# Kernel optimization log

Measured on AMD Instinct MI355X. Metric: run time of the kernel, lower is better.

## Reference

```python
import jax, jax.numpy as jnp
import numpy as np

N = 8192
E = 262144
DIN = 512
DOUT = 256


def setup_inputs() -> dict:
    key = jax.random.key(0)
    k1, k2, k3, k4 = jax.random.split(key, 4)
    x = jax.random.normal(k1, (N, DIN), dtype=jnp.float32)
    edge_index = jax.random.randint(k2, (2, E), 0, N, dtype=jnp.int64)
    edge_weight = jax.random.uniform(k3, (E,), dtype=jnp.float32)
    W = jax.random.normal(k4, (DOUT, DIN), dtype=jnp.float32) * (1.0 / np.sqrt(DIN))
    return {"x": x, "edge_index": edge_index, "edge_weight": edge_weight, "W": W}


def reference(x, edge_index, edge_weight, W):
    n = x.shape[0]
    # Linear(dim_in, dim_out, bias=False): h = x @ W.T  -> [N, DOUT]
    h = x @ W.T
    # Dense adjacency: A[src, dst] += w (to_dense_adj sums duplicate edges)
    src, dst = edge_index[0], edge_index[1]
    A = jnp.zeros((n, n), dtype=x.dtype).at[src, dst].add(edge_weight)
    # degree from A BEFORE self-loops, then +1 from the added eye on degree_matrix
    deg = jnp.sum(A, axis=1) + 1.0
    # sqrt(inverse(diag(deg))) == diag(1/sqrt(deg)); apply as row scaling
    dinv_sqrt = 1.0 / jnp.sqrt(deg)  # [N]
    A = A + jnp.eye(n, dtype=x.dtype)  # self-loops on adjacency
    # x = D^{-1/2} @ (A.T @ (D^{-1/2} @ h))
    h = dinv_sqrt[:, None] * h
    h = A.T @ h
    h = dinv_sqrt[:, None] * h
    return h
```

## Files before the change

kernel.cpp:

```cpp
#include <hip/hip_runtime.h>

static constexpr int DIN = 512;
static constexpr int DOUT = 256;
static constexpr int CAP = 128;

typedef __attribute__((ext_vector_type(8))) short short8;
typedef __attribute__((ext_vector_type(4))) float f32x4;

__device__ inline unsigned short f2bf(float f) {
  unsigned int b = __float_as_uint(f);
  unsigned int r = (b + 0x7fffu + ((b >> 16) & 1u)) >> 16;
  return (unsigned short)r;
}
__device__ inline float bf_lo(unsigned int packed) { return __uint_as_float(packed << 16); }
__device__ inline float bf_hi(unsigned int packed) { return __uint_as_float(packed & 0xffff0000u); }

__device__ inline short8 cvt8(const float4 a, const float4 b) {
  short8 o;
  o[0] = (short)f2bf(a.x); o[1] = (short)f2bf(a.y);
  o[2] = (short)f2bf(a.z); o[3] = (short)f2bf(a.w);
  o[4] = (short)f2bf(b.x); o[5] = (short)f2bf(b.y);
  o[6] = (short)f2bf(b.z); o[7] = (short)f2bf(b.w);
  return o;
}

__global__ __launch_bounds__(256) void k_setup(
    const float* __restrict__ x, const float* __restrict__ W,
    unsigned short* __restrict__ xb, unsigned short* __restrict__ wbb,
    float* __restrict__ deg, int* __restrict__ cursor, int n, long XT, long WT) {
  long gid = (long)blockIdx.x * 256 + threadIdx.x;
  if (gid < XT) {
    const float4* src = (const float4*)(x + gid * 8);
    float4 a = src[0], b = src[1];
    *(short8*)(xb + gid * 8) = cvt8(a, b);
  } else if (gid < XT + WT) {
    long i = gid - XT;
    const float4* src = (const float4*)(W + i * 8);
    float4 a = src[0], b = src[1];
    *(short8*)(wbb + i * 8) = cvt8(a, b);
  } else {
    long i = gid - XT - WT;
    if (i < n) { deg[i] = 1.0f; cursor[i] = 0; }
  }
}

__global__ __launch_bounds__(256) void k_edges(
    const int* __restrict__ ei, const float* __restrict__ ew,
    float* __restrict__ deg, int* __restrict__ cursor,
    uint2* __restrict__ bucket, int E) {
  int e = blockIdx.x * blockDim.x + threadIdx.x;
  if (e < E) {
    int srcv = ei[e];
    int dstv = ei[E + e];
    float w = ew[e];
    atomicAdd(&deg[srcv], w);
    int pos = atomicAdd(&cursor[dstv], 1);
    if (pos < CAP) {
      uint2 v;
      v.x = (unsigned)srcv;
      v.y = __float_as_uint(w);
      bucket[(size_t)dstv * CAP + pos] = v;
    }
  }
}

__global__ __launch_bounds__(256) void k_gemm_mfma(
    const unsigned short* __restrict__ xb, const unsigned short* __restrict__ wbb,
    const float* __restrict__ deg, unsigned short* __restrict__ h1b) {
  const int lane = threadIdx.x & 63;
  const int wv = threadIdx.x >> 6;
  const int bm = blockIdx.x * 16;
  const int colb = wv * 64;
  const int r = lane & 15;
  const int kg = lane >> 4;
  f32x4 acc[4] = {};
  const unsigned short* arow = xb + (size_t)(bm + r) * DIN + kg * 8;
  const unsigned short* brow0 = wbb + (size_t)(colb + r) * DIN + kg * 8;
#pragma unroll
  for (int k0 = 0; k0 < DIN; k0 += 32) {
    short8 av = *(const short8*)(arow + k0);
#pragma unroll
    for (int nt = 0; nt < 4; ++nt) {
      short8 bv = *(const short8*)(brow0 + (size_t)nt * 16 * DIN + k0);
      acc[nt] = __builtin_amdgcn_mfma_f32_16x16x32_bf16(av, bv, acc[nt], 0, 0, 0);
    }
  }
#pragma unroll
  for (int i = 0; i < 4; ++i) {
    int row = bm + kg * 4 + i;
    float sr = __frsqrt_rn(deg[row]);
#pragma unroll
    for (int nt = 0; nt < 4; ++nt) {
      h1b[(size_t)row * DOUT + colb + nt * 16 + r] = f2bf(sr * acc[nt][i]);
    }
  }
}

__global__ __launch_bounds__(256, 4) void k_gather(
    const unsigned short* __restrict__ h1b, const float* __restrict__ deg,
    const int* __restrict__ cursor, const uint2* __restrict__ bucket,
    float* __restrict__ out) {
  const int lane = threadIdx.x & 63;
  const int wv = threadIdx.x >> 6;
  const int dst = blockIdx.x * 4 + wv;
  const int cl = lane & 31;
  const int half = lane >> 5;
  const int cnt = min(cursor[dst], CAP);

  float acc[8] = {};

  for (int base = 0; base < cnt; base += 64) {
    const int c = min(64, cnt - base);
    int sv = 0;
    float wl = 0.f;
    if (lane < c) {
      uint2 ev = bucket[(size_t)dst * CAP + base + lane];
      sv = (int)ev.x;
      wl = __uint_as_float(ev.y);
    }
    const int npair = (c + 1) >> 1;
    int j = 0;
    for (; j + 8 <= npair; j += 8) {
      uint4 rbuf[8];
#pragma unroll
      for (int u = 0; u < 8; ++u) {
        int src = __shfl(sv, 2 * (j + u) + half);
        rbuf[u] = *(const uint4*)(h1b + (size_t)src * DOUT + cl * 8);
      }
#pragma unroll
      for (int u = 0; u < 8; ++u) {
        float w = __shfl(wl, 2 * (j + u) + half);
        acc[0] = fmaf(w, bf_lo(rbuf[u].x), acc[0]);
        acc[1] = fmaf(w, bf_hi(rbuf[u].x), acc[1]);
        acc[2] = fmaf(w, bf_lo(rbuf[u].y), acc[2]);
        acc[3] = fmaf(w, bf_hi(rbuf[u].y), acc[3]);
        acc[4] = fmaf(w, bf_lo(rbuf[u].z), acc[4]);
        acc[5] = fmaf(w, bf_hi(rbuf[u].z), acc[5]);
        acc[6] = fmaf(w, bf_lo(rbuf[u].w), acc[6]);
        acc[7] = fmaf(w, bf_hi(rbuf[u].w), acc[7]);
      }
    }
    for (; j < npair; ++j) {
      int src = __shfl(sv, 2 * j + half);
      float w = __shfl(wl, 2 * j + half);
      uint4 hv = *(const uint4*)(h1b + (size_t)src * DOUT + cl * 8);
      acc[0] = fmaf(w, bf_lo(hv.x), acc[0]);
      acc[1] = fmaf(w, bf_hi(hv.x), acc[1]);
      acc[2] = fmaf(w, bf_lo(hv.y), acc[2]);
      acc[3] = fmaf(w, bf_hi(hv.y), acc[3]);
      acc[4] = fmaf(w, bf_lo(hv.z), acc[4]);
      acc[5] = fmaf(w, bf_hi(hv.z), acc[5]);
      acc[6] = fmaf(w, bf_lo(hv.w), acc[6]);
      acc[7] = fmaf(w, bf_hi(hv.w), acc[7]);
    }
  }

#pragma unroll
  for (int k = 0; k < 8; ++k) acc[k] += __shfl_xor(acc[k], 32);

  if (half == 0) {
    uint4 selfv = *(const uint4*)(h1b + (size_t)dst * DOUT + cl * 8);
    const float sd = __frsqrt_rn(deg[dst]);
    float4 o0v, o1v;
    o0v.x = sd * (bf_lo(selfv.x) + acc[0]);
    o0v.y = sd * (bf_hi(selfv.x) + acc[1]);
    o0v.z = sd * (bf_lo(selfv.y) + acc[2]);
    o0v.w = sd * (bf_hi(selfv.y) + acc[3]);
    o1v.x = sd * (bf_lo(selfv.z) + acc[4]);
    o1v.y = sd * (bf_hi(selfv.z) + acc[5]);
    o1v.z = sd * (bf_lo(selfv.w) + acc[6]);
    o1v.w = sd * (bf_hi(selfv.w) + acc[7]);
    float* op = out + (size_t)dst * DOUT + cl * 8;
    *(float4*)op = o0v;
    *(float4*)(op + 4) = o1v;
  }
}

extern "C" void kernel_launch(void* const* d_in, const int* in_sizes, int n_in,
                              void* d_out, int out_size, void* d_ws, size_t ws_size,
                              hipStream_t stream) {
  const float* x = (const float*)d_in[0];
  const int* ei = (const int*)d_in[1];
  const float* ew = (const float*)d_in[2];
  const float* W = (const float*)d_in[3];
  float* out = (float*)d_out;

  const int n = in_sizes[0] / DIN;
  const int E = in_sizes[2];

  char* p = (char*)d_ws;
  auto alloc = [&](size_t bytes) {
    char* q = p;
    p += (bytes + 255) & ~(size_t)255;
    return q;
  };
  unsigned short* h1b = (unsigned short*)alloc((size_t)n * DOUT * 2);
  unsigned short* xb  = (unsigned short*)alloc((size_t)n * DIN * 2);
  unsigned short* wbb = (unsigned short*)alloc((size_t)DOUT * DIN * 2);
  float* deg   = (float*)alloc((size_t)n * 4);
  int* cursor  = (int*)alloc((size_t)n * 4);
  uint2* bucket = (uint2*)alloc((size_t)n * CAP * 8);

  const long XT = (long)n * DIN / 8;
  const long WT = (long)DOUT * DIN / 8;
  const long setup_threads = XT + WT + n;

  k_setup<<<(int)((setup_threads + 255) / 256), 256, 0, stream>>>(
      x, W, xb, wbb, deg, cursor, n, XT, WT);
  k_edges<<<(E + 255) / 256, 256, 0, stream>>>(ei, ew, deg, cursor, bucket, E);
  k_gemm_mfma<<<n / 16, 256, 0, stream>>>(xb, wbb, deg, h1b);
  k_gather<<<n / 4, 256, 0, stream>>>(h1b, deg, cursor, bucket, out);
}
```

Before: 73.51 us.

## Fuse x bf16 conversion into GEMM and replace setup kernel with memset

Result: no change. 74.05 us (+0.7%).

```diff
diff --git a/kernel.cpp b/kernel.cpp
--- a/kernel.cpp
+++ b/kernel.cpp
@@ -24,48 +24,38 @@
   return o;
 }
 
-__global__ __launch_bounds__(256) void k_setup(
-    const float* __restrict__ x, const float* __restrict__ W,
-    unsigned short* __restrict__ xb, unsigned short* __restrict__ wbb,
-    float* __restrict__ deg, int* __restrict__ cursor, int n, long XT, long WT) {
-  long gid = (long)blockIdx.x * 256 + threadIdx.x;
-  if (gid < XT) {
-    const float4* src = (const float4*)(x + gid * 8);
-    float4 a = src[0], b = src[1];
-    *(short8*)(xb + gid * 8) = cvt8(a, b);
-  } else if (gid < XT + WT) {
-    long i = gid - XT;
-    const float4* src = (const float4*)(W + i * 8);
-    float4 a = src[0], b = src[1];
-    *(short8*)(wbb + i * 8) = cvt8(a, b);
-  } else {
-    long i = gid - XT - WT;
-    if (i < n) { deg[i] = 1.0f; cursor[i] = 0; }
-  }
-}
-
 __global__ __launch_bounds__(256) void k_edges(
     const int* __restrict__ ei, const float* __restrict__ ew,
+    const float* __restrict__ W,
     float* __restrict__ deg, int* __restrict__ cursor,
-    uint2* __restrict__ bucket, int E) {
-  int e = blockIdx.x * blockDim.x + threadIdx.x;
-  if (e < E) {
-    int srcv = ei[e];
-    int dstv = ei[E + e];
-    float w = ew[e];
-    atomicAdd(&deg[srcv], w);
-    int pos = atomicAdd(&cursor[dstv], 1);
-    if (pos < CAP) {
-      uint2 v;
-      v.x = (unsigned)srcv;
-      v.y = __float_as_uint(w);
-      bucket[(size_t)dstv * CAP + pos] = v;
+    uint2* __restrict__ bucket, unsigned short* __restrict__ wbb,
+    int E, int EB) {
+  const int b = blockIdx.x;
+  if (b < EB) {
+    int e = b * 256 + threadIdx.x;
+    if (e < E) {
+      int srcv = ei[e];
+      int dstv = ei[E + e];
+      float w = ew[e];
+      atomicAdd(&deg[srcv], w);
+      int pos = atomicAdd(&cursor[dstv], 1);
+      if (pos < CAP) {
+        uint2 v;
+        v.x = (unsigned)srcv;
+        v.y = __float_as_uint(w);
+        bucket[(size_t)dstv * CAP + pos] = v;
+      }
     }
+  } else {
+    long i = (long)(b - EB) * 256 + threadIdx.x;
+    const float4* src = (const float4*)(W + i * 8);
+    float4 a = src[0], bb = src[1];
+    *(short8*)(wbb + i * 8) = cvt8(a, bb);
   }
 }
 
 __global__ __launch_bounds__(256) void k_gemm_mfma(
-    const unsigned short* __restrict__ xb, const unsigned short* __restrict__ wbb,
+    const float* __restrict__ x, const unsigned short* __restrict__ wbb,
     const float* __restrict__ deg, unsigned short* __restrict__ h1b) {
   const int lane = threadIdx.x & 63;
   const int wv = threadIdx.x >> 6;
@@ -74,11 +64,13 @@
   const int r = lane & 15;
   const int kg = lane >> 4;
   f32x4 acc[4] = {};
-  const unsigned short* arow = xb + (size_t)(bm + r) * DIN + kg * 8;
+  const float* arow = x + (size_t)(bm + r) * DIN + kg * 8;
   const unsigned short* brow0 = wbb + (size_t)(colb + r) * DIN + kg * 8;
 #pragma unroll
   for (int k0 = 0; k0 < DIN; k0 += 32) {
-    short8 av = *(const short8*)(arow + k0);
+    float4 a0 = *(const float4*)(arow + k0);
+    float4 a1 = *(const float4*)(arow + k0 + 4);
+    short8 av = cvt8(a0, a1);
 #pragma unroll
     for (int nt = 0; nt < 4; ++nt) {
       short8 bv = *(const short8*)(brow0 + (size_t)nt * 16 * DIN + k0);
@@ -88,7 +80,7 @@
 #pragma unroll
   for (int i = 0; i < 4; ++i) {
     int row = bm + kg * 4 + i;
-    float sr = __frsqrt_rn(deg[row]);
+    float sr = __frsqrt_rn(1.0f + deg[row]);
 #pragma unroll
     for (int nt = 0; nt < 4; ++nt) {
       h1b[(size_t)row * DOUT + colb + nt * 16 + r] = f2bf(sr * acc[nt][i]);
@@ -107,6 +99,9 @@
   const int half = lane >> 5;
   const int cnt = min(cursor[dst], CAP);
 
+  const uint4 selfv = *(const uint4*)(h1b + (size_t)dst * DOUT + cl * 8);
+  const float sd = __frsqrt_rn(1.0f + deg[dst]);
+
   float acc[8] = {};
 
   for (int base = 0; base < cnt; base += 64) {
@@ -118,9 +113,8 @@
       sv = (int)ev.x;
       wl = __uint_as_float(ev.y);
     }
-    const int npair = (c + 1) >> 1;
-    int j = 0;
-    for (; j + 8 <= npair; j += 8) {
+    const int npair = ((c + 15) >> 4) << 3;
+    for (int j = 0; j < npair; j += 8) {
       uint4 rbuf[8];
 #pragma unroll
       for (int u = 0; u < 8; ++u) {
@@ -140,27 +134,12 @@
         acc[7] = fmaf(w, bf_hi(rbuf[u].w), acc[7]);
       }
     }
-    for (; j < npair; ++j) {
-      int src = __shfl(sv, 2 * j + half);
-      float w = __shfl(wl, 2 * j + half);
-      uint4 hv = *(const uint4*)(h1b + (size_t)src * DOUT + cl * 8);
-      acc[0] = fmaf(w, bf_lo(hv.x), acc[0]);
-      acc[1] = fmaf(w, bf_hi(hv.x), acc[1]);
-      acc[2] = fmaf(w, bf_lo(hv.y), acc[2]);
-      acc[3] = fmaf(w, bf_hi(hv.y), acc[3]);
-      acc[4] = fmaf(w, bf_lo(hv.z), acc[4]);
-      acc[5] = fmaf(w, bf_hi(hv.z), acc[5]);
-      acc[6] = fmaf(w, bf_lo(hv.w), acc[6]);
-      acc[7] = fmaf(w, bf_hi(hv.w), acc[7]);
-    }
   }
 
 #pragma unroll
   for (int k = 0; k < 8; ++k) acc[k] += __shfl_xor(acc[k], 32);
 
   if (half == 0) {
-    uint4 selfv = *(const uint4*)(h1b + (size_t)dst * DOUT + cl * 8);
-    const float sd = __frsqrt_rn(deg[dst]);
     float4 o0v, o1v;
     o0v.x = sd * (bf_lo(selfv.x) + acc[0]);
     o0v.y = sd * (bf_hi(selfv.x) + acc[1]);
@@ -195,19 +174,16 @@
     return q;
   };
   unsigned short* h1b = (unsigned short*)alloc((size_t)n * DOUT * 2);
-  unsigned short* xb  = (unsigned short*)alloc((size_t)n * DIN * 2);
   unsigned short* wbb = (unsigned short*)alloc((size_t)DOUT * DIN * 2);
-  float* deg   = (float*)alloc((size_t)n * 4);
-  int* cursor  = (int*)alloc((size_t)n * 4);
+  float* deg   = (float*)alloc((size_t)n * 4 * 2);
+  int* cursor  = (int*)(deg + n);
   uint2* bucket = (uint2*)alloc((size_t)n * CAP * 8);
 
-  const long XT = (long)n * DIN / 8;
-  const long WT = (long)DOUT * DIN / 8;
-  const long setup_threads = XT + WT + n;
+  const int EB = (E + 255) / 256;
+  const int WB = (DOUT * DIN / 8 + 255) / 256;
 
-  k_setup<<<(int)((setup_threads + 255) / 256), 256, 0, stream>>>(
-      x, W, xb, wbb, deg, cursor, n, XT, WT);
-  k_edges<<<(E + 255) / 256, 256, 0, stream>>>(ei, ew, deg, cursor, bucket, E);
-  k_gemm_mfma<<<n / 16, 256, 0, stream>>>(xb, wbb, deg, h1b);
+  hipMemsetAsync(deg, 0, (size_t)n * 8, stream);
+  k_edges<<<EB + WB, 256, 0, stream>>>(ei, ew, W, deg, cursor, bucket, wbb, E, EB);
+  k_gemm_mfma<<<n / 16, 256, 0, stream>>>(x, wbb, deg, h1b);
   k_gather<<<n / 4, 256, 0, stream>>>(h1b, deg, cursor, bucket, out);
 }
```
